# Performance work log

Measured on AMD Instinct MI355X. Metric: run time of the kernel, lower is better.

Reference implementation:

```python
import jax, jax.numpy as jnp
import numpy as np

B, C, H, W = 16, 64, 64, 64
HEADS = 8

def conv1x1(x, w):
    # x: [B, Cin, H, W], w: [Cout, Cin] -> [B, Cout, H, W]
    return jnp.einsum('oc,bchw->bohw', w, x)

def maxpool2x2(x):
    b, c, h, w = x.shape
    return x.reshape(b, c, h // 2, 2, w // 2, 2).max(axis=(3, 5))

def setup_inputs() -> dict:
    key = jax.random.key(0)
    ks = jax.random.split(key, 6)
    x = jax.random.normal(ks[0], (B, C, H, W), dtype=jnp.float32)
    w_theta = jax.random.normal(ks[1], (C // HEADS, C), dtype=jnp.float32) * 0.05
    w_phi = jax.random.normal(ks[2], (C // HEADS, C), dtype=jnp.float32) * 0.05
    w_g = jax.random.normal(ks[3], (C // 2, C), dtype=jnp.float32) * 0.05
    w_o = jax.random.normal(ks[4], (C, C // 2), dtype=jnp.float32) * 0.05
    gamma = jax.random.normal(ks[5], (), dtype=jnp.float32)
    return {'x': x, 'w_theta': w_theta, 'w_phi': w_phi, 'w_g': w_g, 'w_o': w_o, 'gamma': gamma}

def reference(x, w_theta, w_phi, w_g, w_o, gamma):
    b, c, h, w = x.shape
    n = h * w                      # query length
    m = n // 4                     # kv length after 2x2 maxpool
    theta = conv1x1(x, w_theta).reshape(b, c // HEADS, n)   # [B, C/h, N]
    phi = maxpool2x2(conv1x1(x, w_phi)).reshape(b, c // HEADS, m)  # [B, C/h, M]
    g = maxpool2x2(conv1x1(x, w_g)).reshape(b, c // 2, m)   # [B, C/2, M]
    # attention: theta^T @ phi -> [B, N, M]; NOTE: no 1/sqrt(d) scaling (SAGAN)
    beta = jax.nn.softmax(jnp.einsum('bdn,bdm->bnm', theta, phi), axis=-1)
    # o = g @ beta^T -> [B, C/2, N]
    o = jnp.einsum('bdm,bnm->bdn', g, beta).reshape(b, c // 2, h, w)
    o = conv1x1(o, w_o)            # [B, C, H, W]
    return gamma * o + x
```

## Files before the change

### kernel.cpp

```cpp
#include <hip/hip_runtime.h>
#include <hip/hip_bf16.h>

#define NB 16
#define NC 64
#define NN 4096
#define NM 1024
#define ND 8
#define NG 32

typedef short short8 __attribute__((ext_vector_type(8)));
typedef float floatx4 __attribute__((ext_vector_type(4)));

#define LOG2E 1.44269504f

__device__ __forceinline__ short f2bfs(float f) {
    union { __hip_bfloat16 h; short s; } u;
    u.h = __float2bfloat16(f);
    return u.s;
}
__device__ __forceinline__ unsigned pack2bf(float a, float b) {
    return (unsigned)(unsigned short)f2bfs(a) | ((unsigned)(unsigned short)f2bfs(b) << 16);
}
__device__ __forceinline__ unsigned pk2fast(float a, float b) {
    unsigned ua = __float_as_uint(a) + 0x8000u;
    unsigned ub = __float_as_uint(b) + 0x8000u;
    return __builtin_amdgcn_perm(ub, ua, 0x07060302);
}
__device__ __forceinline__ short8 u4s8(uint4 v) {
    union { uint4 u; short8 s; } c; c.u = v; return c.s;
}

__device__ __forceinline__ uint4 ld_coh(const unsigned* base, size_t u4idx) {
    const unsigned long long* p = (const unsigned long long*)base + u4idx * 2;
    unsigned long long lo = __hip_atomic_load(p,     __ATOMIC_RELAXED,
                                              __HIP_MEMORY_SCOPE_SYSTEM);
    unsigned long long hi = __hip_atomic_load(p + 1, __ATOMIC_RELAXED,
                                              __HIP_MEMORY_SCOPE_SYSTEM);
    return make_uint4((unsigned)lo, (unsigned)(lo >> 32),
                      (unsigned)hi, (unsigned)(hi >> 32));
}
__device__ __forceinline__ void st_coh(unsigned* base, size_t u4idx, uint4 v) {
    unsigned long long* p = (unsigned long long*)base + u4idx * 2;
    __hip_atomic_store(p,     (unsigned long long)v.x | ((unsigned long long)v.y << 32),
                       __ATOMIC_RELAXED, __HIP_MEMORY_SCOPE_SYSTEM);
    __hip_atomic_store(p + 1, (unsigned long long)v.z | ((unsigned long long)v.w << 32),
                       __ATOMIC_RELAXED, __HIP_MEMORY_SCOPE_SYSTEM);
}

#define KG_STEP(CPP0, CPP1, CG_)                                                         \
    {                                                                                    \
        _Pragma("unroll")                                                                \
        for (int qt = 0; qt < 2; ++qt) {                                                 \
            floatx4 s0 = __builtin_amdgcn_mfma_f32_16x16x32_bf16(                        \
                u4s8(CPP0), u4s8(tb[qt]), (floatx4)0.f, 0, 0, 0);                        \
            floatx4 s1 = __builtin_amdgcn_mfma_f32_16x16x32_bf16(                        \
                u4s8(CPP1), u4s8(tb[qt]), (floatx4)0.f, 0, 0, 0);                        \
            float e0[4], e1[4];                                                          \
            _Pragma("unroll")                                                            \
            for (int r = 0; r < 4; ++r) {                                                \
                e0[r] = __builtin_amdgcn_exp2f(s0[r]);                                   \
                e1[r] = __builtin_amdgcn_exp2f(s1[r]);                                   \
            }                                                                            \
            lsum[qt] += ((e0[0] + e0[1]) + (e0[2] + e0[3]))                              \
                      + ((e1[0] + e1[1]) + (e1[2] + e1[3]));                             \
            uint4 pb = make_uint4(pk2fast(e0[0], e0[1]), pk2fast(e0[2], e0[3]),          \
                                  pk2fast(e1[0], e1[1]), pk2fast(e1[2], e1[3]));         \
            _Pragma("unroll")                                                            \
            for (int ct = 0; ct < 4; ++ct)                                               \
                acc[qt][ct] = __builtin_amdgcn_mfma_f32_16x16x32_bf16(                   \
                    u4s8(CG_[ct]), u4s8(pb), acc[qt][ct], 0, 0, 0);                      \
        }                                                                                \
    }

__global__ void init_flags(int* __restrict__ flags)
{
    flags[threadIdx.x] = 0;
}

__global__ __launch_bounds__(256, 2)
void fused_kernel(const float* __restrict__ x,
                  const float* __restrict__ w_theta,
                  const float* __restrict__ w_phi,
                  const float* __restrict__ w_g,
                  const float* __restrict__ w_o,
                  const float* __restrict__ gamma_p,
                  unsigned* __restrict__ phi_ws,
                  unsigned* __restrict__ g2_ws,
                  int* __restrict__ flags,
                  float* __restrict__ out)
{
    __shared__ __align__(16) float smem[16096];
    float* lx   = smem;
    float* lwpT = smem + 8448;
    float* lwgT = smem + 8960;
    float* lwoT = smem + 11072;
    float* lgs  = smem + 13152;
    float* lps  = smem + 14304;
    float* lwt  = smem + 14560;
    float* lth  = smem + 15072;
    uint4* lphi = (uint4*)(smem + 8960);
    float* ltr  = smem;

    const int blk  = blockIdx.x;
    const int xcd  = blk & 7;
    const int slot = blk >> 3;
    const int b    = xcd * 2 + (slot >> 5);
    const int ph   = slot & 31;
    const int t    = threadIdx.x;
    const int w    = t >> 6;
    const int lane = t & 63;
    const int lm   = lane & 15;
    const int quad = lane >> 4;

    for (int i = t; i < 512; i += 256) {
        lwpT[(i & 63) * 8 + (i >> 6)] = w_phi[i];
        lwt[i] = w_theta[i];
    }
    for (int i = t; i < 2048; i += 256) {
        lwgT[(i & 63) * 33 + (i >> 6)] = w_g[i];
        lwoT[(i & 31) * 65 + (i >> 5)] = w_o[i];
    }
    const float* xb = x + (size_t)b * NC * NN + (size_t)ph * 128;
    for (int idx = t; idx < 2048; idx += 256) {
        int c = idx >> 5, i4 = idx & 31;
        ((float4*)(lx + c * 132))[i4] = ((const float4*)(xb + (size_t)c * NN))[i4];
    }
    __syncthreads();

    float4 xr0[4], xr1[4];
    {
        const int l16 = t & 15;
        #pragma unroll
        for (int io = 0; io < 4; ++io) {
            int co = io * 16 + (t >> 4);
            const float* p = &lx[co * 132 + l16 * 8];
            xr0[io] = ((const float4*)p)[0];
            xr1[io] = ((const float4*)p)[1];
        }
    }

    {
        int oc = t >> 3, grp = t & 7;
        float s0[16];
        #pragma unroll
        for (int i = 0; i < 16; ++i) s0[i] = 0.f;
        const float4* xl4 = (const float4*)lx;
        #pragma unroll 4
        for (int c = 0; c < 64; ++c) {
            float4 a0 = xl4[c * 33 + 2 * grp];
            float4 a1 = xl4[c * 33 + 2 * grp + 1];
            float4 b0 = xl4[c * 33 + 16 + 2 * grp];
            float4 b1 = xl4[c * 33 + 17 + 2 * grp];
            float w0 = lwgT[c * 33 + oc];
            s0[0] = fmaf(w0, a0.x, s0[0]);  s0[1] = fmaf(w0, a0.y, s0[1]);
            s0[2] = fmaf(w0, a0.z, s0[2]);  s0[3] = fmaf(w0, a0.w, s0[3]);
            s0[4] = fmaf(w0, a1.x, s0[4]);  s0[5] = fmaf(w0, a1.y, s0[5]);
            s0[6] = fmaf(w0, a1.z, s0[6]);  s0[7] = fmaf(w0, a1.w, s0[7]);
            s0[8] = fmaf(w0, b0.x, s0[8]);  s0[9] = fmaf(w0, b0.y, s0[9]);
            s0[10] = fmaf(w0, b0.z, s0[10]); s0[11] = fmaf(w0, b0.w, s0[11]);
            s0[12] = fmaf(w0, b1.x, s0[12]); s0[13] = fmaf(w0, b1.y, s0[13]);
            s0[14] = fmaf(w0, b1.z, s0[14]); s0[15] = fmaf(w0, b1.w, s0[15]);
        }
        #pragma unroll
        for (int p = 0; p < 4; ++p)
            lgs[oc * 36 + grp * 4 + p] =
                fmaxf(fmaxf(s0[2 * p], s0[2 * p + 1]), fmaxf(s0[8 + 2 * p], s0[9 + 2 * p]));
    }

    {
        int m = t >> 3, oc = t & 7;
        float s0 = 0.f, s1 = 0.f, s2 = 0.f, s3 = 0.f;
        #pragma unroll 4
        for (int c = 0; c < 64; ++c) {
            float wv = lwpT[c * 8 + oc];
            const float* xr = &lx[c * 132];
            s0 = fmaf(wv, xr[2 * m],      s0);
            s1 = fmaf(wv, xr[2 * m + 1],  s1);
            s2 = fmaf(wv, xr[64 + 2 * m], s2);
            s3 = fmaf(wv, xr[65 + 2 * m], s3);
        }
        lps[m * 8 + oc] = fmaxf(fmaxf(s0, s1), fmaxf(s2, s3));
    }

    {
        int qi = t & 127, och = (t >> 7) * 4;
        float th4[4] = {0.f, 0.f, 0.f, 0.f};
        for (int c = 0; c < 64; ++c) {
            float xv = lx[c * 132 + qi];
            #pragma unroll
            for (int o = 0; o < 4; ++o)
                th4[o] = fmaf(lwt[(och + o) * 64 + c], xv, th4[o]);
        }
        *(float4*)&lth[qi * 8 + och] = make_float4(th4[0], th4[1], th4[2], th4[3]);
    }
    __syncthreads();

    {
        int co = t >> 2, sel = t & 3;
        int m0a = 4 * sel, m0b = 16 + 4 * sel;
        float v[8];
        #pragma unroll
        for (int mm = 0; mm < 8; ++mm) v[mm] = 0.f;
        #pragma unroll 4
        for (int c = 0; c < 32; ++c) {
            float wv = lwoT[c * 65 + co];
            float4 ga = *(const float4*)&lgs[c * 36 + m0a];
            float4 gb = *(const float4*)&lgs[c * 36 + m0b];
            v[0] = fmaf(wv, ga.x, v[0]); v[1] = fmaf(wv, ga.y, v[1]);
            v[2] = fmaf(wv, ga.z, v[2]); v[3] = fmaf(wv, ga.w, v[3]);
            v[4] = fmaf(wv, gb.x, v[4]); v[5] = fmaf(wv, gb.y, v[5]);
            v[6] = fmaf(wv, gb.z, v[6]); v[7] = fmaf(wv, gb.w, v[7]);
        }
        uint4 pk;
        pk.x = pack2bf(v[0], v[1]); pk.y = pack2bf(v[2], v[3]);
        pk.z = pack2bf(v[4], v[5]); pk.w = pack2bf(v[6], v[7]);
        int ln = (sel << 4) | (co & 15);
        st_coh(g2_ws, (((size_t)b * 4 + (co >> 4)) * 32 + ph) * 64 + ln, pk);
    }

    if (t < 32) {
        const float* pr = &lps[t * 8];
        uint4 pk;
        pk.x = pack2bf(pr[0], pr[1]); pk.y = pack2bf(pr[2], pr[3]);
        pk.z = pack2bf(pr[4], pr[5]); pk.w = pack2bf(pr[6], pr[7]);
        st_coh(phi_ws, (size_t)b * NM + ph * 32 + t, pk);
    }

    uint4 tb[2];
    #pragma unroll
    for (int qt = 0; qt < 2; ++qt) {
        const float* thp = &lth[(w * 32 + qt * 16 + lm) * 8];
        float4 a = ((const float4*)thp)[0], c4 = ((const float4*)thp)[1];
        uint4 v;
        v.x = pack2bf(a.x * LOG2E, a.y * LOG2E);
        v.y = pack2bf(a.z * LOG2E, a.w * LOG2E);
        v.z = pack2bf(c4.x * LOG2E, c4.y * LOG2E);
        v.w = pack2bf(c4.z * LOG2E, c4.w * LOG2E);
        tb[qt].x = quad == 0 ? v.x : 0u;
        tb[qt].y = quad == 0 ? v.y : 0u;
        tb[qt].z = quad == 0 ? v.z : 0u;
        tb[qt].w = quad == 0 ? v.w : 0u;
    }

    asm volatile("s_waitcnt vmcnt(0)" ::: "memory");
    __syncthreads();
    if (t == 0) {
        __hip_atomic_fetch_add(&flags[b * 32], 1, __ATOMIC_RELAXED,
                               __HIP_MEMORY_SCOPE_AGENT);
        while (__hip_atomic_load(&flags[b * 32], __ATOMIC_RELAXED,
                                 __HIP_MEMORY_SCOPE_AGENT) < 32)
            __builtin_amdgcn_s_sleep(8);
    }
    __syncthreads();

    uint4 gA[4], gB[4];
    #pragma unroll
    for (int ct = 0; ct < 4; ++ct) {
        gA[ct] = ld_coh(g2_ws, (((size_t)b * 4 + ct) * 32 + 0) * 64 + lane);
        gB[ct] = ld_coh(g2_ws, (((size_t)b * 4 + ct) * 32 + 1) * 64 + lane);
    }
    for (int kk = t; kk < NM; kk += 256)
        lphi[kk] = ld_coh(phi_ws, (size_t)b * NM + kk);
    __syncthreads();

    floatx4 acc[2][4];
    #pragma unroll
    for (int qt = 0; qt < 2; ++qt)
        #pragma unroll
        for (int ct = 0; ct < 4; ++ct) acc[qt][ct] = (floatx4)0.f;
    float lsum[2] = {0.f, 0.f};

    uint4 qA0 = lphi[lm],      qA1 = lphi[16 + lm];
    uint4 qB0 = lphi[32 + lm], qB1 = lphi[48 + lm];

    for (int kg2 = 0; kg2 < 16; ++kg2) {
        {
            uint4 c0 = qA0, c1 = qA1;
            uint4 cg[4] = {gA[0], gA[1], gA[2], gA[3]};
            if (kg2 < 15) {
                int nk = 2 * kg2 + 2;
                qA0 = lphi[nk * 32 + lm];
                qA1 = lphi[nk * 32 + 16 + lm];
                #pragma unroll
                for (int ct = 0; ct < 4; ++ct)
                    gA[ct] = ld_coh(g2_ws, (((size_t)b * 4 + ct) * 32 + nk) * 64 + lane);
            }
            KG_STEP(c0, c1, cg);
        }
        {
            uint4 c0 = qB0, c1 = qB1;
            uint4 cg[4] = {gB[0], gB[1], gB[2], gB[3]};
            if (kg2 < 15) {
                int nk = 2 * kg2 + 3;
                qB0 = lphi[nk * 32 + lm];
                qB1 = lphi[nk * 32 + 16 + lm];
                #pragma unroll
                for (int ct = 0; ct < 4; ++ct)
                    gB[ct] = ld_coh(g2_ws, (((size_t)b * 4 + ct) * 32 + nk) * 64 + lane);
            }
            KG_STEP(c0, c1, cg);
        }
    }

    float inv[2];
    {
        float l0 = lsum[0]; l0 += __shfl_xor(l0, 16); l0 += __shfl_xor(l0, 32);
        float l1 = lsum[1]; l1 += __shfl_xor(l1, 16); l1 += __shfl_xor(l1, 32);
        inv[0] = 1.0f / l0; inv[1] = 1.0f / l1;
    }

    const float gamma = gamma_p[0];

    __syncthreads();
    #pragma unroll
    for (int qt = 0; qt < 2; ++qt)
        #pragma unroll
        for (int ct = 0; ct < 4; ++ct)
            #pragma unroll
            for (int r = 0; r < 4; ++r)
                ltr[(ct * 16 + quad * 4 + r) * 140 + w * 32 + qt * 16 + lm]
                    = acc[qt][ct][r] * inv[qt];
    __syncthreads();

    {
        const int l16 = t & 15;
        #pragma unroll
        for (int io = 0; io < 4; ++io) {
            int co = io * 16 + (t >> 4);
            size_t base = ((size_t)b * NC + co) * NN + (size_t)ph * 128 + l16 * 8;
            const float* tr = &ltr[co * 140 + l16 * 8];
            float4 t0 = ((const float4*)tr)[0];
            float4 t1 = ((const float4*)tr)[1];
            float4 o0 = make_float4(fmaf(gamma, t0.x, xr0[io].x), fmaf(gamma, t0.y, xr0[io].y),
                                    fmaf(gamma, t0.z, xr0[io].z), fmaf(gamma, t0.w, xr0[io].w));
            float4 o1 = make_float4(fmaf(gamma, t1.x, xr1[io].x), fmaf(gamma, t1.y, xr1[io].y),
                                    fmaf(gamma, t1.z, xr1[io].z), fmaf(gamma, t1.w, xr1[io].w));
            *(float4*)(out + base)     = o0;
            *(float4*)(out + base + 4) = o1;
        }
    }
}

extern "C" void kernel_launch(void* const* d_in, const int* in_sizes, int n_in,
                              void* d_out, int out_size, void* d_ws, size_t ws_size,
                              hipStream_t stream)
{
    const float* x  = (const float*)d_in[0];
    const float* wt = (const float*)d_in[1];
    const float* wp = (const float*)d_in[2];
    const float* wg = (const float*)d_in[3];
    const float* wo = (const float*)d_in[4];
    const float* gm = (const float*)d_in[5];
    float* out = (float*)d_out;

    unsigned* phi_ws = (unsigned*)d_ws;
    unsigned* g2_ws  = phi_ws + (size_t)NB * NM * ND / 2;
    int* flags = (int*)((char*)d_ws + (size_t)(256 * 1024 + 2 * 1024 * 1024));

    init_flags<<<1, NB * 32, 0, stream>>>(flags);
    fused_kernel<<<NB * 32, 256, 0, stream>>>(x, wt, wp, wg, wo, gm,
                                              phi_ws, g2_ws, flags, out);
}
```

Before: 122.6 us.

## Stage g tiles cooperatively in double-buffered LDS instead of per-wave global loads

```diff
diff --git a/kernel.cpp b/kernel.cpp
--- a/kernel.cpp
+++ b/kernel.cpp
@@ -99,6 +99,7 @@
     float* lwt  = smem + 14560;
     float* lth  = smem + 15072;
     uint4* lphi = (uint4*)(smem + 8960);
+    uint4* lg2  = (uint4*)(smem + 13056);
     float* ltr  = smem;
 
     const int blk  = blockIdx.x;
@@ -253,12 +254,8 @@
     }
     __syncthreads();
 
-    uint4 gA[4], gB[4];
-    #pragma unroll
-    for (int ct = 0; ct < 4; ++ct) {
-        gA[ct] = ld_coh(g2_ws, (((size_t)b * 4 + ct) * 32 + 0) * 64 + lane);
-        gB[ct] = ld_coh(g2_ws, (((size_t)b * 4 + ct) * 32 + 1) * 64 + lane);
-    }
+    const size_t gbase = ((size_t)b * 4 + w) * 32 * 64 + lane;
+    lg2[t] = ld_coh(g2_ws, gbase);
     for (int kk = t; kk < NM; kk += 256)
         lphi[kk] = ld_coh(phi_ws, (size_t)b * NM + kk);
     __syncthreads();
@@ -270,36 +267,20 @@
         for (int ct = 0; ct < 4; ++ct) acc[qt][ct] = (floatx4)0.f;
     float lsum[2] = {0.f, 0.f};
 
-    uint4 qA0 = lphi[lm],      qA1 = lphi[16 + lm];
-    uint4 qB0 = lphi[32 + lm], qB1 = lphi[48 + lm];
-
-    for (int kg2 = 0; kg2 < 16; ++kg2) {
-        {
-            uint4 c0 = qA0, c1 = qA1;
-            uint4 cg[4] = {gA[0], gA[1], gA[2], gA[3]};
-            if (kg2 < 15) {
-                int nk = 2 * kg2 + 2;
-                qA0 = lphi[nk * 32 + lm];
-                qA1 = lphi[nk * 32 + 16 + lm];
-                #pragma unroll
-                for (int ct = 0; ct < 4; ++ct)
-                    gA[ct] = ld_coh(g2_ws, (((size_t)b * 4 + ct) * 32 + nk) * 64 + lane);
-            }
-            KG_STEP(c0, c1, cg);
-        }
-        {
-            uint4 c0 = qB0, c1 = qB1;
-            uint4 cg[4] = {gB[0], gB[1], gB[2], gB[3]};
-            if (kg2 < 15) {
-                int nk = 2 * kg2 + 3;
-                qB0 = lphi[nk * 32 + lm];
-                qB1 = lphi[nk * 32 + 16 + lm];
-                #pragma unroll
-                for (int ct = 0; ct < 4; ++ct)
-                    gB[ct] = ld_coh(g2_ws, (((size_t)b * 4 + ct) * 32 + nk) * 64 + lane);
-            }
-            KG_STEP(c0, c1, cg);
-        }
+    for (int kg = 0; kg < 32; ++kg) {
+        if (kg < 31)
+            lg2[((kg + 1) & 1) * 256 + t] = ld_coh(g2_ws, gbase + (kg + 1) * 64);
+
+        uint4 c0 = lphi[kg * 32 + lm];
+        uint4 c1 = lphi[kg * 32 + 16 + lm];
+        uint4 cg[4];
+        #pragma unroll
+        for (int ct = 0; ct < 4; ++ct)
+            cg[ct] = lg2[(kg & 1) * 256 + ct * 64 + lane];
+
+        KG_STEP(c0, c1, cg);
+
+        __syncthreads();
     }
 
     float inv[2];
@@ -311,7 +292,6 @@
 
     const float gamma = gamma_p[0];
 
-    __syncthreads();
     #pragma unroll
     for (int qt = 0; qt < 2; ++qt)
         #pragma unroll
```

Result: no change. 123.1 us (+0.4%).
